# Kernel optimization log

Measured on AMD Instinct MI355X. Metric: run time of the kernel, lower is better.

The kernel has to match this reference:

```python
import jax, jax.numpy as jnp
import numpy as np

INF = 100000000.0
TOPK = 13
ALPHA = 1
BETA = 6


def box_cxcywh_to_xyxy(b):
    cx, cy, w, h = jnp.split(b, 4, axis=-1)
    return jnp.concatenate([cx - 0.5 * w, cy - 0.5 * h, cx + 0.5 * w, cy + 0.5 * h], axis=-1)


def generalized_box_iou(boxes1, boxes2):
    # boxes1: [N,4] xyxy, boxes2: [G,4] xyxy -> [N,G]
    area1 = (boxes1[:, 2] - boxes1[:, 0]) * (boxes1[:, 3] - boxes1[:, 1])
    area2 = (boxes2[:, 2] - boxes2[:, 0]) * (boxes2[:, 3] - boxes2[:, 1])
    lt = jnp.maximum(boxes1[:, None, :2], boxes2[None, :, :2])
    rb = jnp.minimum(boxes1[:, None, 2:], boxes2[None, :, 2:])
    wh = jnp.clip(rb - lt, 0.0)
    inter = wh[..., 0] * wh[..., 1]
    union = area1[:, None] + area2[None, :] - inter
    iou = inter / union
    lt_e = jnp.minimum(boxes1[:, None, :2], boxes2[None, :, :2])
    rb_e = jnp.maximum(boxes1[:, None, 2:], boxes2[None, :, 2:])
    wh_e = jnp.clip(rb_e - lt_e, 0.0)
    area_e = wh_e[..., 0] * wh_e[..., 1]
    return iou - (area_e - union) / area_e


def _assign_one(cls_logits, bbox_pred, gt_boxes, gt_labels):
    # cls_logits [N,C], bbox_pred [N,4] cxcywh, gt_boxes [G,4] cxcywh, gt_labels [G]
    N = bbox_pred.shape[0]
    G = gt_boxes.shape[0]
    scores = jax.nn.sigmoid(cls_logits)
    overlaps = -generalized_box_iou(box_cxcywh_to_xyxy(bbox_pred), box_cxcywh_to_xyxy(gt_boxes))  # [N,G]
    bbox_scores = scores[:, gt_labels]                       # [N,G] gather per-gt class score
    alignment = bbox_scores ** ALPHA * overlaps ** BETA      # [N,G]
    # per-gt topk over queries
    cand_metrics, cand_idxs = jax.lax.top_k(alignment.T, TOPK)  # [G,K]
    is_pos = cand_metrics > 0
    vals = jnp.take_along_axis(overlaps.T, cand_idxs, axis=1)   # [G,K]
    rows = jnp.broadcast_to(jnp.arange(G)[:, None], (G, TOPK))
    cols = jnp.where(is_pos, cand_idxs, N)  # out-of-bounds col -> dropped
    oinf = jnp.full((G, N), -INF, dtype=overlaps.dtype)
    oinf = oinf.at[rows, cols].set(vals, mode='drop')
    max_overlaps = oinf.max(axis=0)     # [N]
    argmax_overlaps = oinf.argmax(axis=0)
    pos = max_overlaps != -INF
    assigned_gt_inds = jnp.where(pos, argmax_overlaps + 1, 0)
    assign_metrics = jnp.where(pos, alignment[jnp.arange(N), argmax_overlaps], 0.0)
    assigned_labels = jnp.where(pos, gt_labels[argmax_overlaps], -1)
    return assigned_gt_inds, assigned_labels, assign_metrics


def setup_inputs() -> dict:
    key = jax.random.key(0)
    k1, k2, k3, k4 = jax.random.split(key, 4)
    bs, N, C, G = 16, 4000, 80, 300
    return {
        'pred_logits': jax.random.normal(k1, (bs, N, C), dtype=jnp.float32),
        'pred_boxes': jax.random.uniform(k2, (bs, N, 4), dtype=jnp.float32, minval=0.05, maxval=0.95),
        'gt_boxes': jax.random.uniform(k3, (bs, G, 4), dtype=jnp.float32, minval=0.05, maxval=0.95),
        'gt_labels': jax.random.randint(k4, (bs, G), 0, C),
    }


def reference(pred_logits, pred_boxes, gt_boxes, gt_labels):
    # Fixed-shape equivalent of matched_list: assigned_gt_inds[b,q] == 0 means
    # background; k>0 means query q matched to gt k-1 (same semantics as the
    # (valid_query_idx, valid_assigned_gt_inds) pairs in the torch code).
    return jax.vmap(_assign_one)(pred_logits, pred_boxes, gt_boxes, gt_labels)
```

## Files before the change

### kernel.cpp

```cpp
#include <hip/hip_runtime.h>

#define NPRED 4000
#define NGT   300
#define NCLS  80
#define TOPKK 13
#define NCHUNK 63

__device__ __forceinline__ float frcp(float x) { return __builtin_amdgcn_rcpf(x); }
__device__ __forceinline__ float fexp(float x) {
    return __builtin_amdgcn_exp2f(x * 1.44269504088896341f);
}

__device__ __forceinline__ float neg_giou(float4 pb, float gx1, float gy1,
                                          float gx2, float gy2, float garea) {
    float hw = 0.5f * pb.z, hh = 0.5f * pb.w;
    float px1 = pb.x - hw, py1 = pb.y - hh;
    float px2 = pb.x + hw, py2 = pb.y + hh;
    float parea = (px2 - px1) * (py2 - py1);
    float whx = fmaxf(fminf(px2, gx2) - fmaxf(px1, gx1), 0.0f);
    float why = fmaxf(fminf(py2, gy2) - fmaxf(py1, gy1), 0.0f);
    float inter = whx * why;
    float uni = parea + garea - inter;
    float iou = inter * frcp(uni);
    float wex = fmaxf(px2, gx2) - fminf(px1, gx1);
    float wey = fmaxf(py2, gy2) - fminf(py1, gy1);
    float area_e = wex * wey;
    float giou = iou - (area_e - uni) * frcp(area_e);
    return -giou;
}

__device__ __forceinline__ float sigmoid_fast(float x) {
    return frcp(1.0f + fexp(-x));
}

__device__ __forceinline__ float pow6(float x) {
    float x2 = x * x;
    float x4 = x2 * x2;
    return x2 * x4;
}

__device__ __forceinline__ unsigned ord_float(float f) {
    unsigned u = __float_as_uint(f);
    return u ^ ((unsigned)(((int)u) >> 31) | 0x80000000u);
}

__global__ void init_keys(unsigned long long* keys, int n) {
    int i = blockIdx.x * blockDim.x + threadIdx.x;
    if (i < n) keys[i] = 0ULL;
}

__global__ __launch_bounds__(256) void sig_transpose(const float* __restrict__ logits,
                                                     float* __restrict__ st,
                                                     unsigned long long* __restrict__ keys,
                                                     int total_keys) {
    const int tid = threadIdx.x;
    const int gid = blockIdx.x * 256 + tid;
    if (gid < total_keys) keys[gid] = 0ULL;

    const int b = blockIdx.x / NCHUNK;
    const int n0 = (blockIdx.x % NCHUNK) * 64;

    __shared__ float tile[NCLS][64 + 1];

    const float* src = logits + ((size_t)b * NPRED + n0) * NCLS;
    const int lim = (NPRED - n0 < 64 ? NPRED - n0 : 64) * NCLS;
    for (int i = tid; i < 64 * NCLS; i += 256) {
        float v = (i < lim) ? src[i] : 0.0f;
        tile[i % NCLS][i / NCLS] = sigmoid_fast(v);
    }
    __syncthreads();
    float* dst = st + (size_t)b * NCLS * NPRED + n0;
    for (int i = tid; i < 64 * NCLS; i += 256) {
        int c = i >> 6, r = i & 63;
        if (n0 + r < NPRED) dst[(size_t)c * NPRED + r] = tile[c][r];
    }
}

template <bool PRE>
__global__ __launch_bounds__(256) void topk_scatter(const float* __restrict__ logits,
                                                    const float* __restrict__ st,
                                                    const float4* __restrict__ pboxes,
                                                    const float4* __restrict__ gboxes,
                                                    const int* __restrict__ glabels,
                                                    unsigned long long* __restrict__ keys) {
    const int blk = blockIdx.x;
    const int b = blk / NGT;
    const int g = blk - b * NGT;
    const int tid = threadIdx.x;

    __shared__ unsigned s_key[NPRED];
    __shared__ unsigned s_rv[8];
    __shared__ int      s_ri[8];
    __shared__ int      s_win[TOPKK];

    float4 gb = gboxes[b * NGT + g];
    const int lab = glabels[b * NGT + g];
    const float gx1 = gb.x - 0.5f * gb.z;
    const float gy1 = gb.y - 0.5f * gb.w;
    const float gx2 = gb.x + 0.5f * gb.z;
    const float gy2 = gb.y + 0.5f * gb.w;
    const float garea = (gx2 - gx1) * (gy2 - gy1);

    const float* lg = logits + (size_t)b * NPRED * NCLS + lab;
    const float* srow = st + ((size_t)b * NCLS + lab) * NPRED;
    const float4* pbb = pboxes + (size_t)b * NPRED;

    unsigned bv = 0u; int bi = 0x7FFFFFFF;
    #pragma unroll 4
    for (int n = tid; n < NPRED; n += 256) {
        float o = neg_giou(pbb[n], gx1, gy1, gx2, gy2, garea);
        float s = PRE ? srow[n] : sigmoid_fast(lg[(size_t)n * NCLS]);
        unsigned v = ord_float(s * pow6(o));
        s_key[n] = v;
        if (v > bv) { bv = v; bi = n; }
    }

    int nwin = 0;
    for (int k = 0; k < TOPKK; ++k) {
        unsigned rv = bv; int ri = bi;
        #pragma unroll
        for (int off = 32; off > 0; off >>= 1) {
            unsigned v2 = __shfl_down(rv, off, 64);
            int      i2 = __shfl_down(ri, off, 64);
            bool take = (v2 > rv) || (v2 == rv && i2 < ri);
            rv = take ? v2 : rv;
            ri = take ? i2 : ri;
        }
        const int buf = (k & 1) * 4;
        if ((tid & 63) == 0) { s_rv[buf + (tid >> 6)] = rv; s_ri[buf + (tid >> 6)] = ri; }
        __syncthreads();
        unsigned wv = s_rv[buf]; int wi = s_ri[buf];
        #pragma unroll
        for (int w = 1; w < 4; ++w) {
            unsigned v2 = s_rv[buf + w]; int i2 = s_ri[buf + w];
            if (v2 > wv || (v2 == wv && i2 < wi)) { wv = v2; wi = i2; }
        }
        if (wv <= 0x80000000u) break;
        if (tid == 0) s_win[k] = wi;
        nwin = k + 1;
        if (tid == (wi & 255)) {
            s_key[wi] = 0u;
            bv = 0u; bi = 0x7FFFFFFF;
            #pragma unroll 4
            for (int n = tid; n < NPRED; n += 256) {
                unsigned v = s_key[n];
                if (v > bv) { bv = v; bi = n; }
            }
        }
    }
    __syncthreads();

    if (tid < nwin) {
        int wi = s_win[tid];
        float o = neg_giou(pbb[wi], gx1, gy1, gx2, gy2, garea);
        unsigned long long key = ((unsigned long long)ord_float(o) << 32)
                               | (unsigned long long)(0xFFFFFFFFu - (unsigned)g);
        atomicMax(&keys[(size_t)b * NPRED + wi], key);
    }
}

__global__ void finalize(const float* __restrict__ logits,
                         const float4* __restrict__ pboxes,
                         const float4* __restrict__ gboxes,
                         const int* __restrict__ glabels,
                         const unsigned long long* __restrict__ keys,
                         float* __restrict__ out, int total) {
    int i = blockIdx.x * blockDim.x + threadIdx.x;
    if (i >= total) return;
    int b = i / NPRED;
    unsigned long long key = keys[i];
    float o0 = 0.0f, o1 = -1.0f, o2 = 0.0f;
    if (key != 0ULL) {
        int g = (int)(0xFFFFFFFFu - (unsigned)(key & 0xFFFFFFFFull));
        int lab = glabels[b * NGT + g];
        float4 gb = gboxes[b * NGT + g];
        float gx1 = gb.x - 0.5f * gb.z;
        float gy1 = gb.y - 0.5f * gb.w;
        float gx2 = gb.x + 0.5f * gb.z;
        float gy2 = gb.y + 0.5f * gb.w;
        float garea = (gx2 - gx1) * (gy2 - gy1);
        float o = neg_giou(pboxes[i], gx1, gy1, gx2, gy2, garea);
        float s = sigmoid_fast(logits[(size_t)i * NCLS + lab]);
        o0 = (float)(g + 1);
        o1 = (float)lab;
        o2 = s * pow6(o);
    }
    out[i] = o0;
    out[(size_t)total + i] = o1;
    out[(size_t)2 * total + i] = o2;
}

extern "C" void kernel_launch(void* const* d_in, const int* in_sizes, int n_in,
                              void* d_out, int out_size, void* d_ws, size_t ws_size,
                              hipStream_t stream) {
    const float* logits  = (const float*)d_in[0];
    const float4* pboxes = (const float4*)d_in[1];
    const float4* gboxes = (const float4*)d_in[2];
    const int* glabels   = (const int*)d_in[3];

    const int bs = in_sizes[3] / NGT;
    const int total = bs * NPRED;
    unsigned long long* keys = (unsigned long long*)d_ws;
    float* st = (float*)((char*)d_ws + (size_t)total * sizeof(unsigned long long));
    float* out = (float*)d_out;

    const size_t need = (size_t)total * 8 + (size_t)bs * NCLS * NPRED * 4;
    if (ws_size >= need) {
        sig_transpose<<<bs * NCHUNK, 256, 0, stream>>>(logits, st, keys, total);
        topk_scatter<true><<<bs * NGT, 256, 0, stream>>>(logits, st, pboxes, gboxes,
                                                         glabels, keys);
    } else {
        init_keys<<<(total + 255) / 256, 256, 0, stream>>>(keys, total);
        topk_scatter<false><<<bs * NGT, 256, 0, stream>>>(logits, st, pboxes, gboxes,
                                                          glabels, keys);
    }
    finalize<<<(total + 255) / 256, 256, 0, stream>>>(logits, pboxes, gboxes, glabels,
                                                      keys, out, total);
}
```

Before: 150.7 us.

## Per-wave independent top-k with final merge, keep top-2 per thread, vectorize transpose

The top-k selection no longer synchronizes the whole block on every iteration. Each wave finds its own 13 best candidates using xor-shuffle reductions, and wave 0 then merges the 4x13 candidates with shuffles. Each thread now tracks its top-2 values, so it only rescans shared memory after using up both. The sigmoid transpose kernel also switches to float4 loads and stores. The cost is more register state and a more intricate merge step, where tie-breaking correctness depends on the index ordering.

```diff
diff --git a/kernel.cpp b/kernel.cpp
--- a/kernel.cpp
+++ b/kernel.cpp
@@ -59,20 +59,35 @@
 
     const int b = blockIdx.x / NCHUNK;
     const int n0 = (blockIdx.x % NCHUNK) * 64;
+    const int nval = (NPRED - n0 < 64) ? (NPRED - n0) : 64;
 
     __shared__ float tile[NCLS][64 + 1];
 
-    const float* src = logits + ((size_t)b * NPRED + n0) * NCLS;
-    const int lim = (NPRED - n0 < 64 ? NPRED - n0 : 64) * NCLS;
-    for (int i = tid; i < 64 * NCLS; i += 256) {
-        float v = (i < lim) ? src[i] : 0.0f;
-        tile[i % NCLS][i / NCLS] = sigmoid_fast(v);
+    const float4* src = (const float4*)(logits + ((size_t)b * NPRED + n0) * NCLS);
+    #pragma unroll
+    for (int it = 0; it < 5; ++it) {
+        int i4 = tid + it * 256;
+        int p = i4 / 20;
+        int c = i4 * 4 - p * 80;
+        if (p < nval) {
+            float4 v = src[i4];
+            tile[c + 0][p] = sigmoid_fast(v.x);
+            tile[c + 1][p] = sigmoid_fast(v.y);
+            tile[c + 2][p] = sigmoid_fast(v.z);
+            tile[c + 3][p] = sigmoid_fast(v.w);
+        }
     }
     __syncthreads();
-    float* dst = st + (size_t)b * NCLS * NPRED + n0;
-    for (int i = tid; i < 64 * NCLS; i += 256) {
-        int c = i >> 6, r = i & 63;
-        if (n0 + r < NPRED) dst[(size_t)c * NPRED + r] = tile[c][r];
+    float* dstbase = st + (size_t)b * NCLS * NPRED + n0;
+    #pragma unroll
+    for (int it = 0; it < 5; ++it) {
+        int w4 = tid + it * 256;
+        int c = w4 >> 4, r4 = (w4 & 15) * 4;
+        if (r4 < nval) {
+            float4 v = make_float4(tile[c][r4], tile[c][r4 + 1],
+                                   tile[c][r4 + 2], tile[c][r4 + 3]);
+            *(float4*)(dstbase + (size_t)c * NPRED + r4) = v;
+        }
     }
 }
 
@@ -87,11 +102,12 @@
     const int b = blk / NGT;
     const int g = blk - b * NGT;
     const int tid = threadIdx.x;
+    const int wave = tid >> 6;
+    const int lane = tid & 63;
 
     __shared__ unsigned s_key[NPRED];
-    __shared__ unsigned s_rv[8];
-    __shared__ int      s_ri[8];
-    __shared__ int      s_win[TOPKK];
+    __shared__ unsigned s_cv[4][TOPKK];
+    __shared__ int      s_ci[4][TOPKK];
 
     float4 gb = gboxes[b * NGT + g];
     const int lab = glabels[b * NGT + g];
@@ -105,57 +121,71 @@
     const float* srow = st + ((size_t)b * NCLS + lab) * NPRED;
     const float4* pbb = pboxes + (size_t)b * NPRED;
 
-    unsigned bv = 0u; int bi = 0x7FFFFFFF;
+    unsigned b1v = 0u; int b1i = 0x7FFFFFFF;
+    unsigned b2v = 0u; int b2i = 0x7FFFFFFF;
     #pragma unroll 4
     for (int n = tid; n < NPRED; n += 256) {
         float o = neg_giou(pbb[n], gx1, gy1, gx2, gy2, garea);
         float s = PRE ? srow[n] : sigmoid_fast(lg[(size_t)n * NCLS]);
         unsigned v = ord_float(s * pow6(o));
         s_key[n] = v;
-        if (v > bv) { bv = v; bi = n; }
-    }
-
-    int nwin = 0;
+        if (v > b1v)      { b2v = b1v; b2i = b1i; b1v = v; b1i = n; }
+        else if (v > b2v) { b2v = v; b2i = n; }
+    }
+
     for (int k = 0; k < TOPKK; ++k) {
-        unsigned rv = bv; int ri = bi;
+        unsigned rv = b1v; int ri = b1i;
         #pragma unroll
-        for (int off = 32; off > 0; off >>= 1) {
-            unsigned v2 = __shfl_down(rv, off, 64);
-            int      i2 = __shfl_down(ri, off, 64);
-            bool take = (v2 > rv) || (v2 == rv && i2 < ri);
-            rv = take ? v2 : rv;
-            ri = take ? i2 : ri;
-        }
-        const int buf = (k & 1) * 4;
-        if ((tid & 63) == 0) { s_rv[buf + (tid >> 6)] = rv; s_ri[buf + (tid >> 6)] = ri; }
-        __syncthreads();
-        unsigned wv = s_rv[buf]; int wi = s_ri[buf];
-        #pragma unroll
-        for (int w = 1; w < 4; ++w) {
-            unsigned v2 = s_rv[buf + w]; int i2 = s_ri[buf + w];
-            if (v2 > wv || (v2 == wv && i2 < wi)) { wv = v2; wi = i2; }
-        }
-        if (wv <= 0x80000000u) break;
-        if (tid == 0) s_win[k] = wi;
-        nwin = k + 1;
-        if (tid == (wi & 255)) {
-            s_key[wi] = 0u;
-            bv = 0u; bi = 0x7FFFFFFF;
-            #pragma unroll 4
-            for (int n = tid; n < NPRED; n += 256) {
-                unsigned v = s_key[n];
-                if (v > bv) { bv = v; bi = n; }
+        for (int m = 1; m < 64; m <<= 1) {
+            unsigned v2 = __shfl_xor(rv, m, 64);
+            int      i2 = __shfl_xor(ri, m, 64);
+            if (v2 > rv || (v2 == rv && i2 < ri)) { rv = v2; ri = i2; }
+        }
+        if (lane == 0) { s_cv[wave][k] = rv; s_ci[wave][k] = ri; }
+        if (rv <= 0x80000000u) {
+            if (lane == 0)
+                for (int kk = k + 1; kk < TOPKK; ++kk) { s_cv[wave][kk] = 0u; s_ci[wave][kk] = 0x7FFFFFFF; }
+            break;
+        }
+        if (tid == (ri & 255)) {
+            s_key[ri] = 0u;
+            if (b2v != 0u) { b1v = b2v; b1i = b2i; b2v = 0u; b2i = 0x7FFFFFFF; }
+            else {
+                b1v = 0u; b1i = 0x7FFFFFFF;
+                #pragma unroll 4
+                for (int n = tid; n < NPRED; n += 256) {
+                    unsigned v = s_key[n];
+                    if (v > b1v)      { b2v = b1v; b2i = b1i; b1v = v; b1i = n; }
+                    else if (v > b2v) { b2v = v; b2i = n; }
+                }
             }
         }
     }
     __syncthreads();
 
-    if (tid < nwin) {
-        int wi = s_win[tid];
-        float o = neg_giou(pbb[wi], gx1, gy1, gx2, gy2, garea);
-        unsigned long long key = ((unsigned long long)ord_float(o) << 32)
-                               | (unsigned long long)(0xFFFFFFFFu - (unsigned)g);
-        atomicMax(&keys[(size_t)b * NPRED + wi], key);
+    if (wave == 0) {
+        unsigned cv = 0u; int ci = 0x7FFFFFFF;
+        int w = lane >> 4, j = lane & 15;
+        if (j < TOPKK) { cv = s_cv[w][j]; ci = s_ci[w][j]; }
+        int mywin = -1;
+        for (int k = 0; k < TOPKK; ++k) {
+            unsigned wv = cv; int wi = ci;
+            #pragma unroll
+            for (int m = 1; m < 64; m <<= 1) {
+                unsigned v2 = __shfl_xor(wv, m, 64);
+                int      i2 = __shfl_xor(wi, m, 64);
+                if (v2 > wv || (v2 == wv && i2 < wi)) { wv = v2; wi = i2; }
+            }
+            if (wv <= 0x80000000u) break;
+            if (cv == wv && ci == wi) cv = 0u;
+            if (lane == k) mywin = wi;
+        }
+        if (mywin >= 0) {
+            float o = neg_giou(pbb[mywin], gx1, gy1, gx2, gy2, garea);
+            unsigned long long key = ((unsigned long long)ord_float(o) << 32)
+                                   | (unsigned long long)(0xFFFFFFFFu - (unsigned)g);
+            atomicMax(&keys[(size_t)b * NPRED + mywin], key);
+        }
     }
 }
 
```

Measured after the change: 155.2 us. 3.0% more time.
